# Kernel optimization log

Hardware: AMD Instinct MI355X
Metric: run time of the kernel (lower is better)

The kernel has to match this reference:

```python
import jax, jax.numpy as jnp
import numpy as np
from jax import lax

N, GH, GE, LH, LL = 19, 64, 64, 64, 2
B, T = 256, 256


def _normalized_adjacency(A):
    # A: (..., n, n). Add self-loops, symmetric degree normalization.
    n = A.shape[-1]
    A = A + jnp.eye(n, dtype=A.dtype)
    deg = jnp.clip(A.sum(axis=-1), 1e-6, None)  # (..., n)
    dis = deg ** -0.5
    return A * dis[..., :, None] * dis[..., None, :]


def _graph_encoder(A, w1_w, w1_b, w2_w, w2_b):
    # A: (B, T, n, n) -> (B, T, GE). Node features X = A rows.
    An = _normalized_adjacency(A)
    X = jax.nn.relu(An @ (A @ w1_w.T + w1_b))   # (B,T,n,GH)
    X = jax.nn.relu(An @ (X @ w2_w.T + w2_b))   # (B,T,n,GE)
    return X.mean(axis=-2)


def _lstm_layer(x, Wih, Whh, bih, bhh):
    # x: (B, T, D); PyTorch gate order i,f,g,o. Returns (B, T, H).
    Bb = x.shape[0]
    H = Whh.shape[1]
    xg = x @ Wih.T + (bih + bhh)  # precompute input contributions (B,T,4H)

    def step(carry, xt):
        h, c = carry
        gates = xt + h @ Whh.T
        i, f, g, o = jnp.split(gates, 4, axis=-1)
        c = jax.nn.sigmoid(f) * c + jax.nn.sigmoid(i) * jnp.tanh(g)
        h = jax.nn.sigmoid(o) * jnp.tanh(c)
        return (h, c), h

    h0 = jnp.zeros((Bb, H), x.dtype)
    (_, _), hs = lax.scan(step, (h0, h0), jnp.swapaxes(xg, 0, 1))
    return jnp.swapaxes(hs, 0, 1)


def setup_inputs() -> dict:
    key = jax.random.key(0)
    ks = jax.random.split(key, 20)
    s = 0.1
    inp = {
        'conn': jax.random.uniform(ks[0], (B, T, N, N), jnp.float32),
        'mask': jnp.ones((B, T), jnp.int32),
        'w1_w': jax.random.normal(ks[1], (GH, N), jnp.float32) * s,
        'w1_b': jax.random.normal(ks[2], (GH,), jnp.float32) * s,
        'w2_w': jax.random.normal(ks[3], (GE, GH), jnp.float32) * s,
        'w2_b': jax.random.normal(ks[4], (GE,), jnp.float32) * s,
        'lstm_Wih0': jax.random.normal(ks[5], (4 * LH, GE), jnp.float32) * s,
        'lstm_Whh0': jax.random.normal(ks[6], (4 * LH, LH), jnp.float32) * s,
        'lstm_bih0': jax.random.normal(ks[7], (4 * LH,), jnp.float32) * s,
        'lstm_bhh0': jax.random.normal(ks[8], (4 * LH,), jnp.float32) * s,
        'lstm_Wih1': jax.random.normal(ks[9], (4 * LH, LH), jnp.float32) * s,
        'lstm_Whh1': jax.random.normal(ks[10], (4 * LH, LH), jnp.float32) * s,
        'lstm_bih1': jax.random.normal(ks[11], (4 * LH,), jnp.float32) * s,
        'lstm_bhh1': jax.random.normal(ks[12], (4 * LH,), jnp.float32) * s,
        'fc1_w': jax.random.normal(ks[13], (32, LH), jnp.float32) * s,
        'fc1_b': jax.random.normal(ks[14], (32,), jnp.float32) * s,
        'fc2_w': jax.random.normal(ks[15], (2, 32), jnp.float32) * s,
        'fc2_b': jax.random.normal(ks[16], (2,), jnp.float32) * s,
    }
    return inp


def reference(conn, mask, w1_w, w1_b, w2_w, w2_b,
              lstm_Wih0, lstm_Whh0, lstm_bih0, lstm_bhh0,
              lstm_Wih1, lstm_Whh1, lstm_bih1, lstm_bhh1,
              fc1_w, fc1_b, fc2_w, fc2_b):
    emb = _graph_encoder(conn, w1_w, w1_b, w2_w, w2_b)  # (B,T,GE)
    mf = mask.astype(emb.dtype)
    emb = emb * mf[:, :, None]
    out = _lstm_layer(emb, lstm_Wih0, lstm_Whh0, lstm_bih0, lstm_bhh0)
    out = _lstm_layer(out, lstm_Wih1, lstm_Whh1, lstm_bih1, lstm_bhh1)  # (B,T,LH)
    lengths = jnp.clip(mask.sum(axis=1), 1, None)
    last_idx = jnp.clip(lengths - 1, 0, None)  # (B,)
    last_h = jnp.take_along_axis(out, last_idx[:, None, None], axis=1)[:, 0, :]
    h = jax.nn.relu(last_h @ fc1_w.T + fc1_b)
    return h @ fc2_w.T + fc2_b  # (B,2) logits
```

## Files before the change

kernel.cpp:

```cpp
#include <hip/hip_runtime.h>
#include <hip/hip_bf16.h>
#include <math.h>

#define GN 19
#define BB 256
#define TT 256

typedef short short8 __attribute__((ext_vector_type(8)));
typedef float f4 __attribute__((ext_vector_type(4)));

union Frag { int i[4]; short8 s; };

#define LWAIT() __asm__ volatile("s_waitcnt lgkmcnt(0)" ::: "memory")
#define WGBAR() __asm__ volatile("s_waitcnt lgkmcnt(0)\ns_barrier" ::: "memory")

__device__ __forceinline__ int pkbf(float a, float b) {
    __hip_bfloat162 h2 = __float22bfloat162_rn(make_float2(a, b));
    union { __hip_bfloat162 h; int i; } u; u.h = h2; return u.i;
}

__device__ __forceinline__ float rl(float v, int j) {
    return __int_as_float(__builtin_amdgcn_readlane(__float_as_int(v), j));
}
__device__ __forceinline__ float fexp2(float x) { return __builtin_amdgcn_exp2f(x); }
__device__ __forceinline__ float frcp(float x)  { return __builtin_amdgcn_rcpf(x); }
__device__ __forceinline__ float sigm(float x)  { return frcp(1.f + fexp2(-1.4426950408889634f * x)); }
__device__ __forceinline__ float tanha(float x) { float e = fexp2(2.8853900817779268f * x); return 1.f - 2.f * frcp(e + 1.f); }

__global__ __launch_bounds__(64) void encoder_mfma(
    const float* __restrict__ conn,
    const int*   __restrict__ mask,
    const float* __restrict__ w1_w,
    const float* __restrict__ w1_b,
    const float* __restrict__ w2_w,
    const float* __restrict__ w2_b,
    float* __restrict__ emb,
    int num_graphs)
{
    __shared__ float S[2304];
    __shared__ float dis[32];
    __shared__ float ps[256];

    const int t = threadIdx.x;
    const int l15 = t & 15;
    const int quad = t >> 4;

    float km[8];
    #pragma unroll
    for (int j = 0; j < 8; ++j) km[j] = (quad * 8 + j < GN) ? 1.f : 0.f;

    int rr[6], cc[6];
    #pragma unroll
    for (int i = 0; i < 6; ++i) {
        int e = t + 64 * i;
        rr[i] = e / GN;
        cc[i] = e - rr[i] * GN;
    }

    Frag w1F[4];
    #pragma unroll
    for (int nt = 0; nt < 4; ++nt) {
        int n = nt * 16 + l15;
        #pragma unroll
        for (int p = 0; p < 4; ++p) {
            int k0 = quad * 8 + 2 * p, k1 = k0 + 1;
            float a = (k0 < GN) ? w1_w[n * GN + k0] : 0.f;
            float b = (k1 < GN) ? w1_w[n * GN + k1] : 0.f;
            w1F[nt].i[p] = pkbf(a, b);
        }
    }
    Frag w2F[2][4];
    #pragma unroll
    for (int kt = 0; kt < 2; ++kt)
        #pragma unroll
        for (int nt = 0; nt < 4; ++nt) {
            int n = nt * 16 + l15;
            #pragma unroll
            for (int p = 0; p < 4; ++p) {
                int k = kt * 32 + quad * 8 + 2 * p;
                w2F[kt][nt].i[p] = pkbf(w2_w[n * 64 + k], w2_w[n * 64 + k + 1]);
            }
        }
    float b1v[4], b2v[4];
    #pragma unroll
    for (int nt = 0; nt < 4; ++nt) {
        b1v[nt] = w1_b[nt * 16 + l15];
        b2v[nt] = w2_b[nt * 16 + l15];
    }

    float pf[6];
    {
        int g0 = blockIdx.x < num_graphs ? blockIdx.x : 0;
        const float* Ag = conn + (size_t)g0 * (GN * GN);
        #pragma unroll
        for (int i = 0; i < 6; ++i) {
            int e = t + 64 * i;
            if (e < GN * GN) pf[i] = Ag[e];
        }
    }

    #pragma unroll 1
    for (int g = blockIdx.x; g < num_graphs; g += gridDim.x) {
        #pragma unroll
        for (int i = 0; i < 4; ++i) {
            int s = t + 64 * i;
            int row = s >> 3, c4 = s & 7;
            f4 z = {0.f, 0.f, 0.f, 0.f};
            *(f4*)&S[row * 68 + c4 * 4] = z;
        }
        LWAIT();
        #pragma unroll
        for (int i = 0; i < 6; ++i) {
            if (t + 64 * i < GN * GN) S[rr[i] * 68 + cc[i]] = pf[i];
        }
        {
            int gn = g + gridDim.x;
            const float* Ag = conn + (size_t)(gn < num_graphs ? gn : g) * (GN * GN);
            #pragma unroll
            for (int i = 0; i < 6; ++i) {
                int e = t + 64 * i;
                if (e < GN * GN) pf[i] = Ag[e];
            }
        }
        LWAIT();

        if (t < 32) {
            float dv = 0.f;
            if (t < GN) {
                float d = 1.0f;
                #pragma unroll
                for (int c4 = 0; c4 < 8; ++c4) {
                    f4 v = *(f4*)&S[t * 68 + c4 * 4];
                    d += v.x + v.y + v.z + v.w;
                }
                dv = rsqrtf(d);
            }
            dis[t] = dv;
        }
        LWAIT();

        float dk[8];
        {
            f4 v0 = *(f4*)&dis[quad * 8];
            f4 v1 = *(f4*)&dis[quad * 8 + 4];
            dk[0]=v0.x; dk[1]=v0.y; dk[2]=v0.z; dk[3]=v0.w;
            dk[4]=v1.x; dk[5]=v1.y; dk[6]=v1.z; dk[7]=v1.w;
        }
        Frag aF[2], anF[2];
        #pragma unroll
        for (int mt = 0; mt < 2; ++mt) {
            int m = l15 + 16 * mt;
            float dm = dis[m];
            f4 v0 = *(f4*)&S[m * 68 + quad * 8];
            f4 v1 = *(f4*)&S[m * 68 + quad * 8 + 4];
            float av[8] = {v0.x, v0.y, v0.z, v0.w, v1.x, v1.y, v1.z, v1.w};
            float an[8];
            #pragma unroll
            for (int j = 0; j < 8; ++j) {
                int k = quad * 8 + j;
                an[j] = (av[j] + (m == k ? 1.f : 0.f)) * dm * dk[j];
            }
            #pragma unroll
            for (int p = 0; p < 4; ++p) {
                aF[mt].i[p]  = pkbf(av[2*p], av[2*p+1]);
                anF[mt].i[p] = pkbf(an[2*p], an[2*p+1]);
            }
        }
        LWAIT();

        #pragma unroll
        for (int mt = 0; mt < 2; ++mt)
            #pragma unroll
            for (int nt = 0; nt < 4; ++nt) {
                float bb = b1v[nt];
                f4 c = {bb, bb, bb, bb};
                c = __builtin_amdgcn_mfma_f32_16x16x32_bf16(aF[mt].s, w1F[nt].s, c, 0, 0, 0);
                int col = nt * 16 + l15;
                #pragma unroll
                for (int r = 0; r < 4; ++r)
                    S[col * 36 + (mt * 16 + quad * 4 + r)] = c[r];
            }
        LWAIT();

        Frag hF[4];
        #pragma unroll
        for (int nt = 0; nt < 4; ++nt) {
            int n = nt * 16 + l15;
            f4 v0 = *(f4*)&S[n * 36 + quad * 8];
            f4 v1 = *(f4*)&S[n * 36 + quad * 8 + 4];
            float vv[8] = {v0.x, v0.y, v0.z, v0.w, v1.x, v1.y, v1.z, v1.w};
            #pragma unroll
            for (int p = 0; p < 4; ++p)
                hF[nt].i[p] = pkbf(vv[2*p] * km[2*p], vv[2*p+1] * km[2*p+1]);
        }
        LWAIT();

        #pragma unroll
        for (int mt = 0; mt < 2; ++mt)
            #pragma unroll
            for (int nt = 0; nt < 4; ++nt) {
                f4 c = {0.f, 0.f, 0.f, 0.f};
                c = __builtin_amdgcn_mfma_f32_16x16x32_bf16(anF[mt].s, hF[nt].s, c, 0, 0, 0);
                int col = nt * 16 + l15;
                #pragma unroll
                for (int r = 0; r < 4; ++r)
                    S[(mt * 16 + quad * 4 + r) * 68 + col] = fmaxf(c[r], 0.f);
            }
        LWAIT();

        Frag xF[2][2];
        #pragma unroll
        for (int mt = 0; mt < 2; ++mt) {
            int m = l15 + 16 * mt;
            #pragma unroll
            for (int kt = 0; kt < 2; ++kt) {
                f4 v0 = *(f4*)&S[m * 68 + kt * 32 + quad * 8];
                f4 v1 = *(f4*)&S[m * 68 + kt * 32 + quad * 8 + 4];
                xF[mt][kt].i[0] = pkbf(v0.x, v0.y);
                xF[mt][kt].i[1] = pkbf(v0.z, v0.w);
                xF[mt][kt].i[2] = pkbf(v1.x, v1.y);
                xF[mt][kt].i[3] = pkbf(v1.z, v1.w);
            }
        }
        LWAIT();

        #pragma unroll
        for (int mt = 0; mt < 2; ++mt)
            #pragma unroll
            for (int nt = 0; nt < 4; ++nt) {
                float bb = b2v[nt];
                f4 c = {bb, bb, bb, bb};
                c = __builtin_amdgcn_mfma_f32_16x16x32_bf16(xF[mt][0].s, w2F[0][nt].s, c, 0, 0, 0);
                c = __builtin_amdgcn_mfma_f32_16x16x32_bf16(xF[mt][1].s, w2F[1][nt].s, c, 0, 0, 0);
                int col = nt * 16 + l15;
                #pragma unroll
                for (int r = 0; r < 4; ++r)
                    S[col * 36 + (mt * 16 + quad * 4 + r)] = c[r];
            }
        LWAIT();

        #pragma unroll
        for (int nt = 0; nt < 4; ++nt) {
            int n = nt * 16 + l15;
            f4 v0 = *(f4*)&S[n * 36 + quad * 8];
            f4 v1 = *(f4*)&S[n * 36 + quad * 8 + 4];
            float vv[8] = {v0.x, v0.y, v0.z, v0.w, v1.x, v1.y, v1.z, v1.w};
            #pragma unroll
            for (int p = 0; p < 4; ++p)
                hF[nt].i[p] = pkbf(vv[2*p] * km[2*p], vv[2*p+1] * km[2*p+1]);
        }

        float cs[4];
        #pragma unroll
        for (int nt = 0; nt < 4; ++nt) cs[nt] = 0.f;
        #pragma unroll
        for (int mt = 0; mt < 2; ++mt)
            #pragma unroll
            for (int nt = 0; nt < 4; ++nt) {
                f4 c = {0.f, 0.f, 0.f, 0.f};
                c = __builtin_amdgcn_mfma_f32_16x16x32_bf16(anF[mt].s, hF[nt].s, c, 0, 0, 0);
                if (mt == 0) {
                    cs[nt] += fmaxf(c[0], 0.f) + fmaxf(c[1], 0.f)
                            + fmaxf(c[2], 0.f) + fmaxf(c[3], 0.f);
                } else if (quad == 0) {
                    cs[nt] += fmaxf(c[0], 0.f) + fmaxf(c[1], 0.f) + fmaxf(c[2], 0.f);
                }
            }
        #pragma unroll
        for (int nt = 0; nt < 4; ++nt)
            ps[quad * 64 + nt * 16 + l15] = cs[nt];
        LWAIT();
        float tot = ps[t] + ps[64 + t] + ps[128 + t] + ps[192 + t];
        float mf = (float)mask[g];
        emb[(size_t)g * 64 + t] = tot * (1.f / 19.f) * mf;
        LWAIT();
    }
}

__global__ __launch_bounds__(256, 1) void lstm_l0(
    const float* __restrict__ x,
    const float* __restrict__ Wih, const float* __restrict__ Whh,
    const float* __restrict__ bih, const float* __restrict__ bhh,
    float* __restrict__ hseq)
{
    __shared__ float gs[2][256];
    const int tid = threadIdx.x;
    const int w = tid >> 6, l = tid & 63;
    const int b = blockIdx.x;

    float wi[64], wh[64];
    {
        const float4* p = (const float4*)(Wih + tid * 64);
        const float4* q = (const float4*)(Whh + tid * 64);
        #pragma unroll
        for (int j = 0; j < 16; ++j) {
            ((float4*)wi)[j] = p[j];
            ((float4*)wh)[j] = q[j];
        }
    }
    const float bias = bih[tid] + bhh[tid];
    const float* __restrict__ xb = x + (size_t)b * TT * 64;

    float xc;
    {
        float n0 = 0.f, n1 = 0.f, n2 = 0.f, n3 = 0.f;
        #pragma unroll
        for (int j = 0; j < 64; j += 4) {
            n0 = fmaf(xb[j],     wi[j],     n0);
            n1 = fmaf(xb[j + 1], wi[j + 1], n1);
            n2 = fmaf(xb[j + 2], wi[j + 2], n2);
            n3 = fmaf(xb[j + 3], wi[j + 3], n3);
        }
        xc = (n0 + n1) + (n2 + n3);
    }

    float h = 0.f, c = 0.f;

    #pragma unroll 1
    for (int t = 0; t < TT; ++t) {
        const f4* __restrict__ ern = (const f4*)(xb + (t + 1 < TT ? t + 1 : TT - 1) * 64);
        f4 xr[16];
        #pragma unroll
        for (int k = 0; k < 16; ++k) xr[k] = ern[k];

        float a0 = bias + xc, a1 = 0.f, a2 = 0.f, a3 = 0.f;
        #pragma unroll
        for (int j = 0; j < 64; j += 4) {
            a0 = fmaf(rl(h, j),     wh[j],     a0);
            a1 = fmaf(rl(h, j + 1), wh[j + 1], a1);
            a2 = fmaf(rl(h, j + 2), wh[j + 2], a2);
            a3 = fmaf(rl(h, j + 3), wh[j + 3], a3);
        }
        gs[t & 1][tid] = (a0 + a1) + (a2 + a3);
        WGBAR();
        const float* gp = gs[t & 1];
        float gi = gp[l], gf = gp[64 + l], gg = gp[128 + l], go = gp[192 + l];
        c = sigm(gf) * c + sigm(gi) * tanha(gg);
        h = sigm(go) * tanha(c);
        if (w == 0) hseq[((size_t)b * TT + t) * 64 + l] = h;

        float n0 = 0.f, n1 = 0.f, n2 = 0.f, n3 = 0.f;
        #pragma unroll
        for (int k = 0; k < 16; ++k) {
            f4 v = xr[k];
            n0 = fmaf(v.x, wi[4*k],     n0);
            n1 = fmaf(v.y, wi[4*k + 1], n1);
            n2 = fmaf(v.z, wi[4*k + 2], n2);
            n3 = fmaf(v.w, wi[4*k + 3], n3);
        }
        xc = (n0 + n1) + (n2 + n3);
    }
}

__global__ __launch_bounds__(256, 1) void lstm_l1_head(
    const float* __restrict__ x,
    const int*   __restrict__ mask,
    const float* __restrict__ Wih, const float* __restrict__ Whh,
    const float* __restrict__ bih, const float* __restrict__ bhh,
    const float* __restrict__ fc1_w, const float* __restrict__ fc1_b,
    const float* __restrict__ fc2_w, const float* __restrict__ fc2_b,
    float* __restrict__ out)
{
    __shared__ float gs[2][256];
    __shared__ int li_s;
    const int tid = threadIdx.x;
    const int w = tid >> 6, l = tid & 63;
    const int b = blockIdx.x;

    float wi[64], wh[64];
    {
        const float4* p = (const float4*)(Wih + tid * 64);
        const float4* q = (const float4*)(Whh + tid * 64);
        #pragma unroll
        for (int j = 0; j < 16; ++j) {
            ((float4*)wi)[j] = p[j];
            ((float4*)wh)[j] = q[j];
        }
    }
    const float bias = bih[tid] + bhh[tid];

    gs[0][tid] = (float)mask[b * TT + tid];
    __syncthreads();
    if (tid == 0) {
        float s = 0.f;
        for (int t = 0; t < TT; ++t) s += gs[0][t];
        int li = (int)s - 1;
        li = li < 0 ? 0 : (li > TT - 1 ? TT - 1 : li);
        li_s = li;
    }
    __syncthreads();
    const int lastidx = li_s;

    const float* __restrict__ xb = x + (size_t)b * TT * 64;

    float xc;
    {
        float n0 = 0.f, n1 = 0.f, n2 = 0.f, n3 = 0.f;
        #pragma unroll
        for (int j = 0; j < 64; j += 4) {
            n0 = fmaf(xb[j],     wi[j],     n0);
            n1 = fmaf(xb[j + 1], wi[j + 1], n1);
            n2 = fmaf(xb[j + 2], wi[j + 2], n2);
            n3 = fmaf(xb[j + 3], wi[j + 3], n3);
        }
        xc = (n0 + n1) + (n2 + n3);
    }

    float h = 0.f, c = 0.f, hl = 0.f;

    #pragma unroll 1
    for (int t = 0; t < TT; ++t) {
        const f4* __restrict__ ern = (const f4*)(xb + (t + 1 < TT ? t + 1 : TT - 1) * 64);
        f4 xr[16];
        #pragma unroll
        for (int k = 0; k < 16; ++k) xr[k] = ern[k];

        float a0 = bias + xc, a1 = 0.f, a2 = 0.f, a3 = 0.f;
        #pragma unroll
        for (int j = 0; j < 64; j += 4) {
            a0 = fmaf(rl(h, j),     wh[j],     a0);
            a1 = fmaf(rl(h, j + 1), wh[j + 1], a1);
            a2 = fmaf(rl(h, j + 2), wh[j + 2], a2);
            a3 = fmaf(rl(h, j + 3), wh[j + 3], a3);
        }
        gs[t & 1][tid] = (a0 + a1) + (a2 + a3);
        WGBAR();
        const float* gp = gs[t & 1];
        float gi = gp[l], gf = gp[64 + l], gg = gp[128 + l], go = gp[192 + l];
        c = sigm(gf) * c + sigm(gi) * tanha(gg);
        h = sigm(go) * tanha(c);
        if (t == lastidx) hl = h;

        float n0 = 0.f, n1 = 0.f, n2 = 0.f, n3 = 0.f;
        #pragma unroll
        for (int k = 0; k < 16; ++k) {
            f4 v = xr[k];
            n0 = fmaf(v.x, wi[4*k],     n0);
            n1 = fmaf(v.y, wi[4*k + 1], n1);
            n2 = fmaf(v.z, wi[4*k + 2], n2);
            n3 = fmaf(v.w, wi[4*k + 3], n3);
        }
        xc = (n0 + n1) + (n2 + n3);
    }

    __syncthreads();
    if (w == 0 && l < 32) {
        float acc = fc1_b[l];
        const float* fw = fc1_w + l * 64;
        #pragma unroll
        for (int j = 0; j < 64; ++j)
            acc = fmaf(fw[j], rl(hl, j), acc);
        gs[0][l] = fmaxf(acc, 0.f);
    }
    __syncthreads();
    if (w == 0 && l < 2) {
        float acc = fc2_b[l];
        #pragma unroll
        for (int j = 0; j < 32; ++j)
            acc = fmaf(fc2_w[l * 32 + j], gs[0][j], acc);
        out[b * 2 + l] = acc;
    }
}

extern "C" void kernel_launch(void* const* d_in, const int* in_sizes, int n_in,
                              void* d_out, int out_size, void* d_ws, size_t ws_size,
                              hipStream_t stream)
{
    const float* conn  = (const float*)d_in[0];
    const int*   mask  = (const int*)  d_in[1];
    const float* w1_w  = (const float*)d_in[2];
    const float* w1_b  = (const float*)d_in[3];
    const float* w2_w  = (const float*)d_in[4];
    const float* w2_b  = (const float*)d_in[5];
    const float* Wih0  = (const float*)d_in[6];
    const float* Whh0  = (const float*)d_in[7];
    const float* bih0  = (const float*)d_in[8];
    const float* bhh0  = (const float*)d_in[9];
    const float* Wih1  = (const float*)d_in[10];
    const float* Whh1  = (const float*)d_in[11];
    const float* bih1  = (const float*)d_in[12];
    const float* bhh1  = (const float*)d_in[13];
    const float* fc1_w = (const float*)d_in[14];
    const float* fc1_b = (const float*)d_in[15];
    const float* fc2_w = (const float*)d_in[16];
    const float* fc2_b = (const float*)d_in[17];

    float* out = (float*)d_out;
    float* emb   = (float*)d_ws;
    float* h0seq = (float*)d_ws + (size_t)BB * TT * 64;

    const int num_graphs = BB * TT;

    encoder_mfma<<<8192, 64, 0, stream>>>(
        conn, mask, w1_w, w1_b, w2_w, w2_b, emb, num_graphs);

    lstm_l0<<<BB, 256, 0, stream>>>(emb, Wih0, Whh0, bih0, bhh0, h0seq);

    lstm_l1_head<<<BB, 256, 0, stream>>>(
        h0seq, mask, Wih1, Whh1, bih1, bhh1,
        fc1_w, fc1_b, fc2_w, fc2_b, out);
}
```

Baseline: 600.7 us.

## Fuse both LSTM layers into one wavefront-pipelined kernel

```diff
diff --git a/kernel.cpp b/kernel.cpp
--- a/kernel.cpp
+++ b/kernel.cpp
@@ -277,113 +277,46 @@
     }
 }
 
-__global__ __launch_bounds__(256, 1) void lstm_l0(
-    const float* __restrict__ x,
-    const float* __restrict__ Wih, const float* __restrict__ Whh,
-    const float* __restrict__ bih, const float* __restrict__ bhh,
-    float* __restrict__ hseq)
-{
-    __shared__ float gs[2][256];
-    const int tid = threadIdx.x;
-    const int w = tid >> 6, l = tid & 63;
-    const int b = blockIdx.x;
-
-    float wi[64], wh[64];
-    {
-        const float4* p = (const float4*)(Wih + tid * 64);
-        const float4* q = (const float4*)(Whh + tid * 64);
-        #pragma unroll
-        for (int j = 0; j < 16; ++j) {
-            ((float4*)wi)[j] = p[j];
-            ((float4*)wh)[j] = q[j];
-        }
-    }
-    const float bias = bih[tid] + bhh[tid];
-    const float* __restrict__ xb = x + (size_t)b * TT * 64;
-
-    float xc;
-    {
-        float n0 = 0.f, n1 = 0.f, n2 = 0.f, n3 = 0.f;
-        #pragma unroll
-        for (int j = 0; j < 64; j += 4) {
-            n0 = fmaf(xb[j],     wi[j],     n0);
-            n1 = fmaf(xb[j + 1], wi[j + 1], n1);
-            n2 = fmaf(xb[j + 2], wi[j + 2], n2);
-            n3 = fmaf(xb[j + 3], wi[j + 3], n3);
-        }
-        xc = (n0 + n1) + (n2 + n3);
-    }
-
-    float h = 0.f, c = 0.f;
-
-    #pragma unroll 1
-    for (int t = 0; t < TT; ++t) {
-        const f4* __restrict__ ern = (const f4*)(xb + (t + 1 < TT ? t + 1 : TT - 1) * 64);
-        f4 xr[16];
-        #pragma unroll
-        for (int k = 0; k < 16; ++k) xr[k] = ern[k];
-
-        float a0 = bias + xc, a1 = 0.f, a2 = 0.f, a3 = 0.f;
-        #pragma unroll
-        for (int j = 0; j < 64; j += 4) {
-            a0 = fmaf(rl(h, j),     wh[j],     a0);
-            a1 = fmaf(rl(h, j + 1), wh[j + 1], a1);
-            a2 = fmaf(rl(h, j + 2), wh[j + 2], a2);
-            a3 = fmaf(rl(h, j + 3), wh[j + 3], a3);
-        }
-        gs[t & 1][tid] = (a0 + a1) + (a2 + a3);
-        WGBAR();
-        const float* gp = gs[t & 1];
-        float gi = gp[l], gf = gp[64 + l], gg = gp[128 + l], go = gp[192 + l];
-        c = sigm(gf) * c + sigm(gi) * tanha(gg);
-        h = sigm(go) * tanha(c);
-        if (w == 0) hseq[((size_t)b * TT + t) * 64 + l] = h;
-
-        float n0 = 0.f, n1 = 0.f, n2 = 0.f, n3 = 0.f;
-        #pragma unroll
-        for (int k = 0; k < 16; ++k) {
-            f4 v = xr[k];
-            n0 = fmaf(v.x, wi[4*k],     n0);
-            n1 = fmaf(v.y, wi[4*k + 1], n1);
-            n2 = fmaf(v.z, wi[4*k + 2], n2);
-            n3 = fmaf(v.w, wi[4*k + 3], n3);
-        }
-        xc = (n0 + n1) + (n2 + n3);
-    }
-}
-
-__global__ __launch_bounds__(256, 1) void lstm_l1_head(
+__global__ __launch_bounds__(256, 1) void lstm_fused(
     const float* __restrict__ x,
     const int*   __restrict__ mask,
-    const float* __restrict__ Wih, const float* __restrict__ Whh,
-    const float* __restrict__ bih, const float* __restrict__ bhh,
+    const float* __restrict__ Wih0, const float* __restrict__ Whh0,
+    const float* __restrict__ bih0, const float* __restrict__ bhh0,
+    const float* __restrict__ Wih1, const float* __restrict__ Whh1,
+    const float* __restrict__ bih1, const float* __restrict__ bhh1,
     const float* __restrict__ fc1_w, const float* __restrict__ fc1_b,
     const float* __restrict__ fc2_w, const float* __restrict__ fc2_b,
     float* __restrict__ out)
 {
-    __shared__ float gs[2][256];
+    __shared__ float gs0[2][256];
+    __shared__ float gs1[2][256];
     __shared__ int li_s;
     const int tid = threadIdx.x;
     const int w = tid >> 6, l = tid & 63;
     const int b = blockIdx.x;
 
-    float wi[64], wh[64];
+    float wi0[64], wh0[64], wi1[64], wh1[64];
     {
-        const float4* p = (const float4*)(Wih + tid * 64);
-        const float4* q = (const float4*)(Whh + tid * 64);
+        const float4* p0 = (const float4*)(Wih0 + tid * 64);
+        const float4* q0 = (const float4*)(Whh0 + tid * 64);
+        const float4* p1 = (const float4*)(Wih1 + tid * 64);
+        const float4* q1 = (const float4*)(Whh1 + tid * 64);
         #pragma unroll
         for (int j = 0; j < 16; ++j) {
-            ((float4*)wi)[j] = p[j];
-            ((float4*)wh)[j] = q[j];
-        }
-    }
-    const float bias = bih[tid] + bhh[tid];
-
-    gs[0][tid] = (float)mask[b * TT + tid];
+            ((float4*)wi0)[j] = p0[j];
+            ((float4*)wh0)[j] = q0[j];
+            ((float4*)wi1)[j] = p1[j];
+            ((float4*)wh1)[j] = q1[j];
+        }
+    }
+    const float bias0 = bih0[tid] + bhh0[tid];
+    const float bias1 = bih1[tid] + bhh1[tid];
+
+    gs0[0][tid] = (float)mask[b * TT + tid];
     __syncthreads();
     if (tid == 0) {
         float s = 0.f;
-        for (int t = 0; t < TT; ++t) s += gs[0][t];
+        for (int t = 0; t < TT; ++t) s += gs0[0][t];
         int li = (int)s - 1;
         li = li < 0 ? 0 : (li > TT - 1 ? TT - 1 : li);
         li_s = li;
@@ -393,54 +326,88 @@
 
     const float* __restrict__ xb = x + (size_t)b * TT * 64;
 
-    float xc;
+    float xc0;
     {
         float n0 = 0.f, n1 = 0.f, n2 = 0.f, n3 = 0.f;
         #pragma unroll
         for (int j = 0; j < 64; j += 4) {
-            n0 = fmaf(xb[j],     wi[j],     n0);
-            n1 = fmaf(xb[j + 1], wi[j + 1], n1);
-            n2 = fmaf(xb[j + 2], wi[j + 2], n2);
-            n3 = fmaf(xb[j + 3], wi[j + 3], n3);
-        }
-        xc = (n0 + n1) + (n2 + n3);
-    }
-
-    float h = 0.f, c = 0.f, hl = 0.f;
+            n0 = fmaf(xb[j],     wi0[j],     n0);
+            n1 = fmaf(xb[j + 1], wi0[j + 1], n1);
+            n2 = fmaf(xb[j + 2], wi0[j + 2], n2);
+            n3 = fmaf(xb[j + 3], wi0[j + 3], n3);
+        }
+        xc0 = (n0 + n1) + (n2 + n3);
+    }
+
+    float h0 = 0.f, c0 = 0.f;
+    float h1 = 0.f, c1 = 0.f;
+    float hl = 0.f;
 
     #pragma unroll 1
-    for (int t = 0; t < TT; ++t) {
-        const f4* __restrict__ ern = (const f4*)(xb + (t + 1 < TT ? t + 1 : TT - 1) * 64);
+    for (int t = 0; t <= TT; ++t) {
+        const bool do0 = (t < TT);
+        const bool do1 = (t >= 1);
+
         f4 xr[16];
-        #pragma unroll
-        for (int k = 0; k < 16; ++k) xr[k] = ern[k];
-
-        float a0 = bias + xc, a1 = 0.f, a2 = 0.f, a3 = 0.f;
+        if (do0) {
+            const f4* __restrict__ ern =
+                (const f4*)(xb + (t + 1 < TT ? t + 1 : TT - 1) * 64);
+            #pragma unroll
+            for (int k = 0; k < 16; ++k) xr[k] = ern[k];
+        }
+
+        float a0 = bias0 + xc0, a1 = 0.f, a2 = 0.f, a3 = 0.f;
+        float p0 = bias1, p1 = 0.f, p2 = 0.f, p3 = 0.f;
+        float q0 = 0.f, q1 = 0.f, q2 = 0.f, q3 = 0.f;
         #pragma unroll
         for (int j = 0; j < 64; j += 4) {
-            a0 = fmaf(rl(h, j),     wh[j],     a0);
-            a1 = fmaf(rl(h, j + 1), wh[j + 1], a1);
-            a2 = fmaf(rl(h, j + 2), wh[j + 2], a2);
-            a3 = fmaf(rl(h, j + 3), wh[j + 3], a3);
-        }
-        gs[t & 1][tid] = (a0 + a1) + (a2 + a3);
+            float h0a = rl(h0, j),     h0b = rl(h0, j + 1);
+            float h0c = rl(h0, j + 2), h0d = rl(h0, j + 3);
+            a0 = fmaf(h0a, wh0[j],     a0);
+            a1 = fmaf(h0b, wh0[j + 1], a1);
+            a2 = fmaf(h0c, wh0[j + 2], a2);
+            a3 = fmaf(h0d, wh0[j + 3], a3);
+            p0 = fmaf(h0a, wi1[j],     p0);
+            p1 = fmaf(h0b, wi1[j + 1], p1);
+            p2 = fmaf(h0c, wi1[j + 2], p2);
+            p3 = fmaf(h0d, wi1[j + 3], p3);
+            float h1a = rl(h1, j),     h1b = rl(h1, j + 1);
+            float h1c = rl(h1, j + 2), h1d = rl(h1, j + 3);
+            q0 = fmaf(h1a, wh1[j],     q0);
+            q1 = fmaf(h1b, wh1[j + 1], q1);
+            q2 = fmaf(h1c, wh1[j + 2], q2);
+            q3 = fmaf(h1d, wh1[j + 3], q3);
+        }
+        if (do0) gs0[t & 1][tid] = (a0 + a1) + (a2 + a3);
+        if (do1) gs1[t & 1][tid] = ((p0 + p1) + (p2 + p3)) + ((q0 + q1) + (q2 + q3));
         WGBAR();
-        const float* gp = gs[t & 1];
-        float gi = gp[l], gf = gp[64 + l], gg = gp[128 + l], go = gp[192 + l];
-        c = sigm(gf) * c + sigm(gi) * tanha(gg);
-        h = sigm(go) * tanha(c);
-        if (t == lastidx) hl = h;
-
-        float n0 = 0.f, n1 = 0.f, n2 = 0.f, n3 = 0.f;
-        #pragma unroll
-        for (int k = 0; k < 16; ++k) {
-            f4 v = xr[k];
-            n0 = fmaf(v.x, wi[4*k],     n0);
-            n1 = fmaf(v.y, wi[4*k + 1], n1);
-            n2 = fmaf(v.z, wi[4*k + 2], n2);
-            n3 = fmaf(v.w, wi[4*k + 3], n3);
-        }
-        xc = (n0 + n1) + (n2 + n3);
+
+        if (do0) {
+            const float* gp = gs0[t & 1];
+            float gi = gp[l], gf = gp[64 + l], gg = gp[128 + l], go = gp[192 + l];
+            c0 = sigm(gf) * c0 + sigm(gi) * tanha(gg);
+            h0 = sigm(go) * tanha(c0);
+        }
+        if (do1) {
+            const float* gp = gs1[t & 1];
+            float gi = gp[l], gf = gp[64 + l], gg = gp[128 + l], go = gp[192 + l];
+            c1 = sigm(gf) * c1 + sigm(gi) * tanha(gg);
+            h1 = sigm(go) * tanha(c1);
+            if (t - 1 == lastidx) hl = h1;
+        }
+
+        if (do0) {
+            float n0 = 0.f, n1 = 0.f, n2 = 0.f, n3 = 0.f;
+            #pragma unroll
+            for (int k = 0; k < 16; ++k) {
+                f4 v = xr[k];
+                n0 = fmaf(v.x, wi0[4*k],     n0);
+                n1 = fmaf(v.y, wi0[4*k + 1], n1);
+                n2 = fmaf(v.z, wi0[4*k + 2], n2);
+                n3 = fmaf(v.w, wi0[4*k + 3], n3);
+            }
+            xc0 = (n0 + n1) + (n2 + n3);
+        }
     }
 
     __syncthreads();
@@ -450,14 +417,14 @@
         #pragma unroll
         for (int j = 0; j < 64; ++j)
             acc = fmaf(fw[j], rl(hl, j), acc);
-        gs[0][l] = fmaxf(acc, 0.f);
+        gs0[0][l] = fmaxf(acc, 0.f);
     }
     __syncthreads();
     if (w == 0 && l < 2) {
         float acc = fc2_b[l];
         #pragma unroll
         for (int j = 0; j < 32; ++j)
-            acc = fmaf(fc2_w[l * 32 + j], gs[0][j], acc);
+            acc = fmaf(fc2_w[l * 32 + j], gs0[0][j], acc);
         out[b * 2 + l] = acc;
     }
 }
@@ -486,17 +453,14 @@
     const float* fc2_b = (const float*)d_in[17];
 
     float* out = (float*)d_out;
-    float* emb   = (float*)d_ws;
-    float* h0seq = (float*)d_ws + (size_t)BB * TT * 64;
+    float* emb = (float*)d_ws;
 
     const int num_graphs = BB * TT;
 
     encoder_mfma<<<8192, 64, 0, stream>>>(
         conn, mask, w1_w, w1_b, w2_w, w2_b, emb, num_graphs);
 
-    lstm_l0<<<BB, 256, 0, stream>>>(emb, Wih0, Whh0, bih0, bhh0, h0seq);
-
-    lstm_l1_head<<<BB, 256, 0, stream>>>(
-        h0seq, mask, Wih1, Whh1, bih1, bhh1,
+    lstm_fused<<<BB, 256, 0, stream>>>(
+        emb, mask, Wih0, Whh0, bih0, bhh0, Wih1, Whh1, bih1, bhh1,
         fc1_w, fc1_b, fc2_w, fc2_b, out);
 }
```

After: 1.048 ms. 74.5% more time.

## Split LSTM gate dot products across two thread halves per block

Applied to the files above, without the earlier changes.

```diff
diff --git a/kernel.cpp b/kernel.cpp
--- a/kernel.cpp
+++ b/kernel.cpp
@@ -277,35 +277,38 @@
     }
 }
 
-__global__ __launch_bounds__(256, 1) void lstm_l0(
+__global__ __launch_bounds__(512, 2) void lstm_l0(
     const float* __restrict__ x,
     const float* __restrict__ Wih, const float* __restrict__ Whh,
     const float* __restrict__ bih, const float* __restrict__ bhh,
     float* __restrict__ hseq)
 {
-    __shared__ float gs[2][256];
+    __shared__ __align__(16) float gs[2][512];
     const int tid = threadIdx.x;
-    const int w = tid >> 6, l = tid & 63;
+    const int r = tid & 255;
+    const int s = tid >> 8;
+    const int l = tid & 63;
     const int b = blockIdx.x;
-
-    float wi[64], wh[64];
+    const int so = s * 32;
+
+    float wi[32], wh[32];
     {
-        const float4* p = (const float4*)(Wih + tid * 64);
-        const float4* q = (const float4*)(Whh + tid * 64);
-        #pragma unroll
-        for (int j = 0; j < 16; ++j) {
+        const float4* p = (const float4*)(Wih + r * 64 + so);
+        const float4* q = (const float4*)(Whh + r * 64 + so);
+        #pragma unroll
+        for (int j = 0; j < 8; ++j) {
             ((float4*)wi)[j] = p[j];
             ((float4*)wh)[j] = q[j];
         }
     }
-    const float bias = bih[tid] + bhh[tid];
-    const float* __restrict__ xb = x + (size_t)b * TT * 64;
+    const float bias = (s == 0) ? (bih[r] + bhh[r]) : 0.f;
+    const float* __restrict__ xb = x + (size_t)b * TT * 64 + so;
 
     float xc;
     {
         float n0 = 0.f, n1 = 0.f, n2 = 0.f, n3 = 0.f;
         #pragma unroll
-        for (int j = 0; j < 64; j += 4) {
+        for (int j = 0; j < 32; j += 4) {
             n0 = fmaf(xb[j],     wi[j],     n0);
             n1 = fmaf(xb[j + 1], wi[j + 1], n1);
             n2 = fmaf(xb[j + 2], wi[j + 2], n2);
@@ -319,40 +322,55 @@
     #pragma unroll 1
     for (int t = 0; t < TT; ++t) {
         const f4* __restrict__ ern = (const f4*)(xb + (t + 1 < TT ? t + 1 : TT - 1) * 64);
-        f4 xr[16];
-        #pragma unroll
-        for (int k = 0; k < 16; ++k) xr[k] = ern[k];
+        f4 xr0 = ern[0], xr1 = ern[1], xr2 = ern[2], xr3 = ern[3],
+           xr4 = ern[4], xr5 = ern[5], xr6 = ern[6], xr7 = ern[7];
 
         float a0 = bias + xc, a1 = 0.f, a2 = 0.f, a3 = 0.f;
         #pragma unroll
-        for (int j = 0; j < 64; j += 4) {
-            a0 = fmaf(rl(h, j),     wh[j],     a0);
-            a1 = fmaf(rl(h, j + 1), wh[j + 1], a1);
-            a2 = fmaf(rl(h, j + 2), wh[j + 2], a2);
-            a3 = fmaf(rl(h, j + 3), wh[j + 3], a3);
-        }
-        gs[t & 1][tid] = (a0 + a1) + (a2 + a3);
+        for (int j = 0; j < 32; j += 4) {
+            a0 = fmaf(rl(h, so + j),     wh[j],     a0);
+            a1 = fmaf(rl(h, so + j + 1), wh[j + 1], a1);
+            a2 = fmaf(rl(h, so + j + 2), wh[j + 2], a2);
+            a3 = fmaf(rl(h, so + j + 3), wh[j + 3], a3);
+        }
+        gs[t & 1][(r << 1) | s] = (a0 + a1) + (a2 + a3);
         WGBAR();
+
         const float* gp = gs[t & 1];
-        float gi = gp[l], gf = gp[64 + l], gg = gp[128 + l], go = gp[192 + l];
+        float2 vi = *(const float2*)&gp[l * 2];
+        float2 vf = *(const float2*)&gp[(64 + l) * 2];
+        float2 vg = *(const float2*)&gp[(128 + l) * 2];
+        float2 vo = *(const float2*)&gp[(192 + l) * 2];
+        float gi = vi.x + vi.y, gf = vf.x + vf.y;
+        float gg = vg.x + vg.y, go = vo.x + vo.y;
+
+        float n0 = 0.f, n1 = 0.f, n2 = 0.f, n3 = 0.f;
+        n0 = fmaf(xr0.x, wi[0],  n0); n1 = fmaf(xr0.y, wi[1],  n1);
+        n2 = fmaf(xr0.z, wi[2],  n2); n3 = fmaf(xr0.w, wi[3],  n3);
+        n0 = fmaf(xr1.x, wi[4],  n0); n1 = fmaf(xr1.y, wi[5],  n1);
+        n2 = fmaf(xr1.z, wi[6],  n2); n3 = fmaf(xr1.w, wi[7],  n3);
+        n0 = fmaf(xr2.x, wi[8],  n0); n1 = fmaf(xr2.y, wi[9],  n1);
+        n2 = fmaf(xr2.z, wi[10], n2); n3 = fmaf(xr2.w, wi[11], n3);
+        n0 = fmaf(xr3.x, wi[12], n0); n1 = fmaf(xr3.y, wi[13], n1);
+        n2 = fmaf(xr3.z, wi[14], n2); n3 = fmaf(xr3.w, wi[15], n3);
+        n0 = fmaf(xr4.x, wi[16], n0); n1 = fmaf(xr4.y, wi[17], n1);
+        n2 = fmaf(xr4.z, wi[18], n2); n3 = fmaf(xr4.w, wi[19], n3);
+        n0 = fmaf(xr5.x, wi[20], n0); n1 = fmaf(xr5.y, wi[21], n1);
+        n2 = fmaf(xr5.z, wi[22], n2); n3 = fmaf(xr5.w, wi[23], n3);
+        n0 = fmaf(xr6.x, wi[24], n0); n1 = fmaf(xr6.y, wi[25], n1);
+        n2 = fmaf(xr6.z, wi[26], n2); n3 = fmaf(xr6.w, wi[27], n3);
+        n0 = fmaf(xr7.x, wi[28], n0); n1 = fmaf(xr7.y, wi[29], n1);
+        n2 = fmaf(xr7.z, wi[30], n2); n3 = fmaf(xr7.w, wi[31], n3);
+        float xcn = (n0 + n1) + (n2 + n3);
+
         c = sigm(gf) * c + sigm(gi) * tanha(gg);
         h = sigm(go) * tanha(c);
-        if (w == 0) hseq[((size_t)b * TT + t) * 64 + l] = h;
-
-        float n0 = 0.f, n1 = 0.f, n2 = 0.f, n3 = 0.f;
-        #pragma unroll
-        for (int k = 0; k < 16; ++k) {
-            f4 v = xr[k];
-            n0 = fmaf(v.x, wi[4*k],     n0);
-            n1 = fmaf(v.y, wi[4*k + 1], n1);
-            n2 = fmaf(v.z, wi[4*k + 2], n2);
-            n3 = fmaf(v.w, wi[4*k + 3], n3);
-        }
-        xc = (n0 + n1) + (n2 + n3);
+        if (tid < 64) hseq[((size_t)b * TT + t) * 64 + l] = h;
+        xc = xcn;
     }
 }
 
-__global__ __launch_bounds__(256, 1) void lstm_l1_head(
+__global__ __launch_bounds__(512, 2) void lstm_l1_head(
     const float* __restrict__ x,
     const int*   __restrict__ mask,
     const float* __restrict__ Wih, const float* __restrict__ Whh,
@@ -361,43 +379,46 @@
     const float* __restrict__ fc2_w, const float* __restrict__ fc2_b,
     float* __restrict__ out)
 {
-    __shared__ float gs[2][256];
+    __shared__ __align__(16) float gs[2][512];
     __shared__ int li_s;
     const int tid = threadIdx.x;
-    const int w = tid >> 6, l = tid & 63;
+    const int r = tid & 255;
+    const int s = tid >> 8;
+    const int l = tid & 63;
     const int b = blockIdx.x;
-
-    float wi[64], wh[64];
+    const int so = s * 32;
+
+    float wi[32], wh[32];
     {
-        const float4* p = (const float4*)(Wih + tid * 64);
-        const float4* q = (const float4*)(Whh + tid * 64);
-        #pragma unroll
-        for (int j = 0; j < 16; ++j) {
+        const float4* p = (const float4*)(Wih + r * 64 + so);
+        const float4* q = (const float4*)(Whh + r * 64 + so);
+        #pragma unroll
+        for (int j = 0; j < 8; ++j) {
             ((float4*)wi)[j] = p[j];
             ((float4*)wh)[j] = q[j];
         }
     }
-    const float bias = bih[tid] + bhh[tid];
-
-    gs[0][tid] = (float)mask[b * TT + tid];
+    const float bias = (s == 0) ? (bih[r] + bhh[r]) : 0.f;
+
+    if (tid < 256) gs[0][tid] = (float)mask[b * TT + tid];
     __syncthreads();
     if (tid == 0) {
-        float s = 0.f;
-        for (int t = 0; t < TT; ++t) s += gs[0][t];
-        int li = (int)s - 1;
+        float sm = 0.f;
+        for (int t = 0; t < TT; ++t) sm += gs[0][t];
+        int li = (int)sm - 1;
         li = li < 0 ? 0 : (li > TT - 1 ? TT - 1 : li);
         li_s = li;
     }
     __syncthreads();
     const int lastidx = li_s;
 
-    const float* __restrict__ xb = x + (size_t)b * TT * 64;
+    const float* __restrict__ xb = x + (size_t)b * TT * 64 + so;
 
     float xc;
     {
         float n0 = 0.f, n1 = 0.f, n2 = 0.f, n3 = 0.f;
         #pragma unroll
-        for (int j = 0; j < 64; j += 4) {
+        for (int j = 0; j < 32; j += 4) {
             n0 = fmaf(xb[j],     wi[j],     n0);
             n1 = fmaf(xb[j + 1], wi[j + 1], n1);
             n2 = fmaf(xb[j + 2], wi[j + 2], n2);
@@ -411,40 +432,55 @@
     #pragma unroll 1
     for (int t = 0; t < TT; ++t) {
         const f4* __restrict__ ern = (const f4*)(xb + (t + 1 < TT ? t + 1 : TT - 1) * 64);
-        f4 xr[16];
-        #pragma unroll
-        for (int k = 0; k < 16; ++k) xr[k] = ern[k];
+        f4 xr0 = ern[0], xr1 = ern[1], xr2 = ern[2], xr3 = ern[3],
+           xr4 = ern[4], xr5 = ern[5], xr6 = ern[6], xr7 = ern[7];
 
         float a0 = bias + xc, a1 = 0.f, a2 = 0.f, a3 = 0.f;
         #pragma unroll
-        for (int j = 0; j < 64; j += 4) {
-            a0 = fmaf(rl(h, j),     wh[j],     a0);
-            a1 = fmaf(rl(h, j + 1), wh[j + 1], a1);
-            a2 = fmaf(rl(h, j + 2), wh[j + 2], a2);
-            a3 = fmaf(rl(h, j + 3), wh[j + 3], a3);
-        }
-        gs[t & 1][tid] = (a0 + a1) + (a2 + a3);
+        for (int j = 0; j < 32; j += 4) {
+            a0 = fmaf(rl(h, so + j),     wh[j],     a0);
+            a1 = fmaf(rl(h, so + j + 1), wh[j + 1], a1);
+            a2 = fmaf(rl(h, so + j + 2), wh[j + 2], a2);
+            a3 = fmaf(rl(h, so + j + 3), wh[j + 3], a3);
+        }
+        gs[t & 1][(r << 1) | s] = (a0 + a1) + (a2 + a3);
         WGBAR();
+
         const float* gp = gs[t & 1];
-        float gi = gp[l], gf = gp[64 + l], gg = gp[128 + l], go = gp[192 + l];
+        float2 vi = *(const float2*)&gp[l * 2];
+        float2 vf = *(const float2*)&gp[(64 + l) * 2];
+        float2 vg = *(const float2*)&gp[(128 + l) * 2];
+        float2 vo = *(const float2*)&gp[(192 + l) * 2];
+        float gi = vi.x + vi.y, gf = vf.x + vf.y;
+        float gg = vg.x + vg.y, go = vo.x + vo.y;
+
+        float n0 = 0.f, n1 = 0.f, n2 = 0.f, n3 = 0.f;
+        n0 = fmaf(xr0.x, wi[0],  n0); n1 = fmaf(xr0.y, wi[1],  n1);
+        n2 = fmaf(xr0.z, wi[2],  n2); n3 = fmaf(xr0.w, wi[3],  n3);
+        n0 = fmaf(xr1.x, wi[4],  n0); n1 = fmaf(xr1.y, wi[5],  n1);
+        n2 = fmaf(xr1.z, wi[6],  n2); n3 = fmaf(xr1.w, wi[7],  n3);
+        n0 = fmaf(xr2.x, wi[8],  n0); n1 = fmaf(xr2.y, wi[9],  n1);
+        n2 = fmaf(xr2.z, wi[10], n2); n3 = fmaf(xr2.w, wi[11], n3);
+        n0 = fmaf(xr3.x, wi[12], n0); n1 = fmaf(xr3.y, wi[13], n1);
+        n2 = fmaf(xr3.z, wi[14], n2); n3 = fmaf(xr3.w, wi[15], n3);
+        n0 = fmaf(xr4.x, wi[16], n0); n1 = fmaf(xr4.y, wi[17], n1);
+        n2 = fmaf(xr4.z, wi[18], n2); n3 = fmaf(xr4.w, wi[19], n3);
+        n0 = fmaf(xr5.x, wi[20], n0); n1 = fmaf(xr5.y, wi[21], n1);
+        n2 = fmaf(xr5.z, wi[22], n2); n3 = fmaf(xr5.w, wi[23], n3);
+        n0 = fmaf(xr6.x, wi[24], n0); n1 = fmaf(xr6.y, wi[25], n1);
+        n2 = fmaf(xr6.z, wi[26], n2); n3 = fmaf(xr6.w, wi[27], n3);
+        n0 = fmaf(xr7.x, wi[28], n0); n1 = fmaf(xr7.y, wi[29], n1);
+        n2 = fmaf(xr7.z, wi[30], n2); n3 = fmaf(xr7.w, wi[31], n3);
+        float xcn = (n0 + n1) + (n2 + n3);
+
         c = sigm(gf) * c + sigm(gi) * tanha(gg);
         h = sigm(go) * tanha(c);
         if (t == lastidx) hl = h;
-
-        float n0 = 0.f, n1 = 0.f, n2 = 0.f, n3 = 0.f;
-        #pragma unroll
-        for (int k = 0; k < 16; ++k) {
-            f4 v = xr[k];
-            n0 = fmaf(v.x, wi[4*k],     n0);
-            n1 = fmaf(v.y, wi[4*k + 1], n1);
-            n2 = fmaf(v.z, wi[4*k + 2], n2);
-            n3 = fmaf(v.w, wi[4*k + 3], n3);
-        }
-        xc = (n0 + n1) + (n2 + n3);
+        xc = xcn;
     }
 
     __syncthreads();
-    if (w == 0 && l < 32) {
+    if (tid < 32) {
         float acc = fc1_b[l];
         const float* fw = fc1_w + l * 64;
         #pragma unroll
@@ -453,7 +489,7 @@
         gs[0][l] = fmaxf(acc, 0.f);
     }
     __syncthreads();
-    if (w == 0 && l < 2) {
+    if (tid < 2) {
         float acc = fc2_b[l];
         #pragma unroll
         for (int j = 0; j < 32; ++j)
@@ -494,9 +530,9 @@
     encoder_mfma<<<8192, 64, 0, stream>>>(
         conn, mask, w1_w, w1_b, w2_w, w2_b, emb, num_graphs);
 
-    lstm_l0<<<BB, 256, 0, stream>>>(emb, Wih0, Whh0, bih0, bhh0, h0seq);
-
-    lstm_l1_head<<<BB, 256, 0, stream>>>(
+    lstm_l0<<<BB, 512, 0, stream>>>(emb, Wih0, Whh0, bih0, bhh0, h0seq);
+
+    lstm_l1_head<<<BB, 512, 0, stream>>>(
         h0seq, mask, Wih1, Whh1, bih1, bhh1,
         fc1_w, fc1_b, fc2_w, fc2_b, out);
 }
```

Result: slower. 774.0 us (+28.8%).

## Hoist LSTM input projections into parallel GEMM kernels ahead of recurrence

Applied to the files above, without the earlier changes.

```diff
diff --git a/kernel.cpp b/kernel.cpp
--- a/kernel.cpp
+++ b/kernel.cpp
@@ -277,7 +277,166 @@
     }
 }
 
-__global__ __launch_bounds__(256, 1) void lstm_l0(
+__global__ __launch_bounds__(256, 4) void xg_gemm(
+    const float* __restrict__ xin,
+    const float* __restrict__ Wih,
+    float* __restrict__ xg)
+{
+    const int tid = threadIdx.x;
+    float wi[64];
+    {
+        const float4* p = (const float4*)(Wih + tid * 64);
+        #pragma unroll
+        for (int j = 0; j < 16; ++j) ((float4*)wi)[j] = p[j];
+    }
+    const int row0 = blockIdx.x * 32;
+
+    #pragma unroll 2
+    for (int rr = 0; rr < 32; ++rr) {
+        const float* __restrict__ xr = xin + (size_t)(row0 + rr) * 64;
+        float n0 = 0.f, n1 = 0.f, n2 = 0.f, n3 = 0.f;
+        #pragma unroll
+        for (int j = 0; j < 64; j += 4) {
+            n0 = fmaf(xr[j],     wi[j],     n0);
+            n1 = fmaf(xr[j + 1], wi[j + 1], n1);
+            n2 = fmaf(xr[j + 2], wi[j + 2], n2);
+            n3 = fmaf(xr[j + 3], wi[j + 3], n3);
+        }
+        xg[(size_t)(row0 + rr) * 256 + tid] = (n0 + n1) + (n2 + n3);
+    }
+}
+
+__global__ __launch_bounds__(256, 1) void lstm_rec0(
+    const float* __restrict__ xg,
+    const float* __restrict__ Whh,
+    const float* __restrict__ bih, const float* __restrict__ bhh,
+    float* __restrict__ hseq)
+{
+    __shared__ float gs[2][256];
+    const int tid = threadIdx.x;
+    const int w = tid >> 6, l = tid & 63;
+    const int b = blockIdx.x;
+
+    float wh[64];
+    {
+        const float4* q = (const float4*)(Whh + tid * 64);
+        #pragma unroll
+        for (int j = 0; j < 16; ++j) ((float4*)wh)[j] = q[j];
+    }
+    const float bias = bih[tid] + bhh[tid];
+    const float* __restrict__ xgb = xg + (size_t)b * TT * 256 + tid;
+
+    float xc  = xgb[0];
+    float xn1 = xgb[256];
+    float h = 0.f, c = 0.f;
+
+    #pragma unroll 1
+    for (int t = 0; t < TT; ++t) {
+        float xn2 = xgb[(size_t)(t + 2 < TT ? t + 2 : TT - 1) * 256];
+
+        float a0 = bias + xc, a1 = 0.f, a2 = 0.f, a3 = 0.f;
+        #pragma unroll
+        for (int j = 0; j < 64; j += 4) {
+            a0 = fmaf(rl(h, j),     wh[j],     a0);
+            a1 = fmaf(rl(h, j + 1), wh[j + 1], a1);
+            a2 = fmaf(rl(h, j + 2), wh[j + 2], a2);
+            a3 = fmaf(rl(h, j + 3), wh[j + 3], a3);
+        }
+        gs[t & 1][tid] = (a0 + a1) + (a2 + a3);
+        WGBAR();
+
+        const float* gp = gs[t & 1];
+        float gi = gp[l], gf = gp[64 + l], gg = gp[128 + l], go = gp[192 + l];
+        c = sigm(gf) * c + sigm(gi) * tanha(gg);
+        h = sigm(go) * tanha(c);
+        if (w == 0) hseq[((size_t)b * TT + t) * 64 + l] = h;
+        xc = xn1; xn1 = xn2;
+    }
+}
+
+__global__ __launch_bounds__(256, 1) void lstm_rec1_head(
+    const float* __restrict__ xg,
+    const int*   __restrict__ mask,
+    const float* __restrict__ Whh,
+    const float* __restrict__ bih, const float* __restrict__ bhh,
+    const float* __restrict__ fc1_w, const float* __restrict__ fc1_b,
+    const float* __restrict__ fc2_w, const float* __restrict__ fc2_b,
+    float* __restrict__ out)
+{
+    __shared__ float gs[2][256];
+    __shared__ int li_s;
+    const int tid = threadIdx.x;
+    const int w = tid >> 6, l = tid & 63;
+    const int b = blockIdx.x;
+
+    float wh[64];
+    {
+        const float4* q = (const float4*)(Whh + tid * 64);
+        #pragma unroll
+        for (int j = 0; j < 16; ++j) ((float4*)wh)[j] = q[j];
+    }
+    const float bias = bih[tid] + bhh[tid];
+
+    gs[0][tid] = (float)mask[b * TT + tid];
+    __syncthreads();
+    if (tid == 0) {
+        float sm = 0.f;
+        for (int t = 0; t < TT; ++t) sm += gs[0][t];
+        int li = (int)sm - 1;
+        li = li < 0 ? 0 : (li > TT - 1 ? TT - 1 : li);
+        li_s = li;
+    }
+    __syncthreads();
+    const int lastidx = li_s;
+
+    const float* __restrict__ xgb = xg + (size_t)b * TT * 256 + tid;
+    float xc  = xgb[0];
+    float xn1 = xgb[256];
+    float h = 0.f, c = 0.f, hl = 0.f;
+
+    #pragma unroll 1
+    for (int t = 0; t < TT; ++t) {
+        float xn2 = xgb[(size_t)(t + 2 < TT ? t + 2 : TT - 1) * 256];
+
+        float a0 = bias + xc, a1 = 0.f, a2 = 0.f, a3 = 0.f;
+        #pragma unroll
+        for (int j = 0; j < 64; j += 4) {
+            a0 = fmaf(rl(h, j),     wh[j],     a0);
+            a1 = fmaf(rl(h, j + 1), wh[j + 1], a1);
+            a2 = fmaf(rl(h, j + 2), wh[j + 2], a2);
+            a3 = fmaf(rl(h, j + 3), wh[j + 3], a3);
+        }
+        gs[t & 1][tid] = (a0 + a1) + (a2 + a3);
+        WGBAR();
+
+        const float* gp = gs[t & 1];
+        float gi = gp[l], gf = gp[64 + l], gg = gp[128 + l], go = gp[192 + l];
+        c = sigm(gf) * c + sigm(gi) * tanha(gg);
+        h = sigm(go) * tanha(c);
+        if (t == lastidx) hl = h;
+        xc = xn1; xn1 = xn2;
+    }
+
+    __syncthreads();
+    if (w == 0 && l < 32) {
+        float acc = fc1_b[l];
+        const float* fw = fc1_w + l * 64;
+        #pragma unroll
+        for (int j = 0; j < 64; ++j)
+            acc = fmaf(fw[j], rl(hl, j), acc);
+        gs[0][l] = fmaxf(acc, 0.f);
+    }
+    __syncthreads();
+    if (w == 0 && l < 2) {
+        float acc = fc2_b[l];
+        #pragma unroll
+        for (int j = 0; j < 32; ++j)
+            acc = fmaf(fc2_w[l * 32 + j], gs[0][j], acc);
+        out[b * 2 + l] = acc;
+    }
+}
+
+__global__ __launch_bounds__(256, 1) void lstm_l0_fb(
     const float* __restrict__ x,
     const float* __restrict__ Wih, const float* __restrict__ Whh,
     const float* __restrict__ bih, const float* __restrict__ bhh,
@@ -352,7 +511,7 @@
     }
 }
 
-__global__ __launch_bounds__(256, 1) void lstm_l1_head(
+__global__ __launch_bounds__(256, 1) void lstm_l1_head_fb(
     const float* __restrict__ x,
     const int*   __restrict__ mask,
     const float* __restrict__ Wih, const float* __restrict__ Whh,
@@ -486,17 +645,31 @@
     const float* fc2_b = (const float*)d_in[17];
 
     float* out = (float*)d_out;
-    float* emb   = (float*)d_ws;
-    float* h0seq = (float*)d_ws + (size_t)BB * TT * 64;
-
     const int num_graphs = BB * TT;
+
+    const size_t embF = (size_t)BB * TT * 64;
+    const size_t xgF  = (size_t)BB * TT * 256;
+    const size_t needBytes = (embF * 2 + xgF) * sizeof(float);
+
+    float* emb = (float*)d_ws;
 
     encoder_mfma<<<8192, 64, 0, stream>>>(
         conn, mask, w1_w, w1_b, w2_w, w2_b, emb, num_graphs);
 
-    lstm_l0<<<BB, 256, 0, stream>>>(emb, Wih0, Whh0, bih0, bhh0, h0seq);
-
-    lstm_l1_head<<<BB, 256, 0, stream>>>(
-        h0seq, mask, Wih1, Whh1, bih1, bhh1,
-        fc1_w, fc1_b, fc2_w, fc2_b, out);
-}
+    if (ws_size >= needBytes) {
+        float* xg    = emb + embF;
+        float* h0seq = xg + xgF;
+
+        xg_gemm<<<num_graphs / 32, 256, 0, stream>>>(emb, Wih0, xg);
+        lstm_rec0<<<BB, 256, 0, stream>>>(xg, Whh0, bih0, bhh0, h0seq);
+        xg_gemm<<<num_graphs / 32, 256, 0, stream>>>(h0seq, Wih1, xg);
+        lstm_rec1_head<<<BB, 256, 0, stream>>>(
+            xg, mask, Whh1, bih1, bhh1, fc1_w, fc1_b, fc2_w, fc2_b, out);
+    } else {
+        float* h0seq = emb + embF;
+        lstm_l0_fb<<<BB, 256, 0, stream>>>(emb, Wih0, Whh0, bih0, bhh0, h0seq);
+        lstm_l1_head_fb<<<BB, 256, 0, stream>>>(
+            h0seq, mask, Wih1, Whh1, bih1, bhh1,
+            fc1_w, fc1_b, fc2_w, fc2_b, out);
+    }
+}
```

After: 961.2 us. 60.0% more time.
